# Kernel tuning notes

Measured on AMD Instinct MI355X. Metric: run time of the kernel, lower is better.

## Reference

```python
import jax, jax.numpy as jnp
import numpy as np

N_NODES = 100000
N_EDGES = 1600000
D_IN = 128
D_OUT = 128
NEG_SLOPE = 0.01  # torch F.leaky_relu default


def setup_inputs() -> dict:
    key = jax.random.key(0)
    k1, k2, k3, k4, k5 = jax.random.split(key, 5)
    h = jax.random.normal(k1, (N_NODES, D_IN), dtype=jnp.float32)
    # nn.Linear default init scale ~ 1/sqrt(fan_in)
    W = jax.random.normal(k2, (D_IN, D_OUT), dtype=jnp.float32) / np.sqrt(D_IN)
    attn_w = jax.random.normal(k3, (2 * D_OUT,), dtype=jnp.float32) / np.sqrt(2 * D_OUT)
    edge_src = jax.random.randint(k4, (N_EDGES,), 0, N_NODES, dtype=jnp.int32)
    edge_dst = jax.random.randint(k5, (N_EDGES,), 0, N_NODES, dtype=jnp.int32)
    return {"h": h, "W": W, "attn_w": attn_w, "edge_src": edge_src, "edge_dst": edge_dst}


def reference(h, W, attn_w, edge_src, edge_dst):
    n = h.shape[0]
    d = W.shape[1]
    z = h @ W                                   # [N, d]
    # attention_func(cat([z_src, z_dst])) == z_src @ a[:d] + z_dst @ a[d:]
    s_src = z @ attn_w[:d]                      # [N]
    s_dst = z @ attn_w[d:]                      # [N]
    e = jax.nn.leaky_relu(s_src[edge_src] + s_dst[edge_dst], NEG_SLOPE)  # [E]
    # segment softmax over incoming edges of each dst node
    m = jax.ops.segment_max(e, edge_dst, num_segments=n)   # [N], -inf for empty
    ex = jnp.exp(e - m[edge_dst])                           # [E]
    denom = jax.ops.segment_sum(ex, edge_dst, num_segments=n)  # [N]
    alpha = ex / denom[edge_dst]                             # [E]
    # weighted neighbor sum: sum_j alpha_ij * z_j
    out = jax.ops.segment_sum(alpha[:, None] * z[edge_src], edge_dst, num_segments=n)
    return out
```

## Files before the change

### kernel.cpp

```cpp
#include <hip/hip_runtime.h>

#define D 128
#define NEG_SLOPE 0.01f
#define BSHIFT 7
#define B1 1024
#define SCHUNK 4096
#define SLOT 2560

typedef __attribute__((ext_vector_type(8))) short short8;
typedef __attribute__((ext_vector_type(4))) float floatx4;

__device__ __forceinline__ unsigned f2bf_rne(float x) {
    unsigned u = __float_as_uint(x);
    return (u + 0x7fffu + ((u >> 16) & 1u)) >> 16;
}
#define BF_LO(u) __uint_as_float((u) << 16)
#define BF_HI(u) __uint_as_float((u) & 0xffff0000u)

__global__ void init_gcur(int* __restrict__ gcur) {
    const int i = threadIdx.x;
    gcur[i] = i * SLOT;
}

__global__ __launch_bounds__(256) void prep_wfrag(const float* __restrict__ W,
                                                  unsigned short* __restrict__ whi,
                                                  unsigned short* __restrict__ wlo) {
    const int idx = blockIdx.x * 256 + threadIdx.x;
    const int j    = idx & 7;
    const int lane = (idx >> 3) & 63;
    const int tk   = idx >> 9;
    const int kk = tk & 3, ct = tk >> 2;
    const int k = kk * 32 + (lane >> 4) * 8 + j;
    const int n = ct * 16 + (lane & 15);
    const float x = W[k * D + n];
    const unsigned hi = f2bf_rne(x);
    const float hf = __uint_as_float(hi << 16);
    whi[idx] = (unsigned short)hi;
    wlo[idx] = (unsigned short)(__float_as_uint(x - hf) >> 16);
}

__global__ __launch_bounds__(1024) void sort_scatter(const int* __restrict__ esrc,
                                                     const int* __restrict__ edst,
                                                     int* __restrict__ gcur,
                                                     int* __restrict__ pairs, int E) {
    __shared__ int cnt[B1], exc[B1], gbs[B1], cur[B1];
    __shared__ int spk[SCHUNK];
    __shared__ unsigned short sbkt[SCHUNK];
    const int t = threadIdx.x;
    cnt[t] = 0; cur[t] = 0;
    __syncthreads();

    const int e0 = blockIdx.x * SCHUNK;
    const int n  = min(SCHUNK, E - e0);

    int pk[4], bk[4];
#pragma unroll
    for (int k = 0; k < 4; ++k) {
        const int i = t + k * 1024;
        if (i < n) {
            const int d = edst[e0 + i];
            const int s = esrc[e0 + i];
            bk[k] = d >> BSHIFT;
            pk[k] = (s << BSHIFT) | (d & 127);
            atomicAdd(&cnt[bk[k]], 1);
        } else {
            bk[k] = -1;
        }
    }
    __syncthreads();

    exc[t] = cnt[t];
    __syncthreads();
    for (int off = 1; off < B1; off <<= 1) {
        int v = (t >= off) ? exc[t - off] : 0;
        __syncthreads();
        exc[t] += v;
        __syncthreads();
    }
    const int myexc = exc[t] - cnt[t];
    exc[t] = myexc;
    if (cnt[t] > 0) gbs[t] = atomicAdd(&gcur[t], cnt[t]);
    __syncthreads();

#pragma unroll
    for (int k = 0; k < 4; ++k) {
        if (bk[k] >= 0) {
            const int p = exc[bk[k]] + atomicAdd(&cur[bk[k]], 1);
            spk[p]  = pk[k];
            sbkt[p] = (unsigned short)bk[k];
        }
    }
    __syncthreads();

    for (int i = t; i < n; i += 1024) {
        const int b = sbkt[i];
        const int pos = gbs[b] + (i - exc[b]);
        if (pos < (b + 1) * SLOT) pairs[pos] = spk[i];
    }
}

__global__ __launch_bounds__(256) void fine_build(const int* __restrict__ pairs,
                                                  const int* __restrict__ gcur,
                                                  int* __restrict__ beg,
                                                  int* __restrict__ ncnt,
                                                  int* __restrict__ adj, int N) {
    __shared__ int cnt[128], sc[128], cur[128];
    const int b = blockIdx.x;
    const int base = b << BSHIFT;
    const int nd = min(128, N - base);
    const int t = threadIdx.x;
    const int s0 = b * SLOT;
    const int e1 = min(gcur[b], s0 + SLOT);
    if (t < 128) { cnt[t] = 0; cur[t] = 0; }
    __syncthreads();
    for (int i = s0 + t; i < e1; i += 256)
        atomicAdd(&cnt[pairs[i] & 127], 1);
    __syncthreads();
    if (t < 128) sc[t] = cnt[t];
    __syncthreads();
    for (int off = 1; off < 128; off <<= 1) {
        int v = (t < 128 && t >= off) ? sc[t - off] : 0;
        __syncthreads();
        if (t < 128) sc[t] += v;
        __syncthreads();
    }
    if (t < nd) {
        beg[base + t]  = s0 + sc[t] - cnt[t];
        ncnt[base + t] = cnt[t];
    }
    __syncthreads();
    for (int i = s0 + t; i < e1; i += 256) {
        const int pkv = pairs[i];
        const int d = pkv & 127;
        const int pos = s0 + (sc[d] - cnt[d]) + atomicAdd(&cur[d], 1);
        adj[pos] = pkv >> BSHIFT;
    }
}

__global__ __launch_bounds__(256) void gemm_zs(const float* __restrict__ h,
                                               const unsigned short* __restrict__ whi,
                                               const unsigned short* __restrict__ wlo,
                                               const float* __restrict__ aw,
                                               unsigned short* __restrict__ z,
                                               float* __restrict__ s_src,
                                               float* __restrict__ s_dst, int N) {
    const int t = threadIdx.x;
    const int lane = t & 63, quad = lane >> 4, l16 = lane & 15;
    const int rowbase = blockIdx.x * 64 + (t >> 6) * 16;
    const int arow = min(rowbase + l16, N - 1);
    const float* __restrict__ hrow = h + (size_t)arow * D;

    floatx4 acc[8];
#pragma unroll
    for (int ct = 0; ct < 8; ++ct) acc[ct] = (floatx4){0.f, 0.f, 0.f, 0.f};

#pragma unroll
    for (int kk = 0; kk < 4; ++kk) {
        const int k0 = kk * 32 + quad * 8;
        float4 x0 = *(const float4*)&hrow[k0];
        float4 x1 = *(const float4*)&hrow[k0 + 4];
        float xs[8] = {x0.x, x0.y, x0.z, x0.w, x1.x, x1.y, x1.z, x1.w};
        union { short8 v; unsigned short u[8]; } ahi, alo;
#pragma unroll
        for (int i = 0; i < 8; ++i) {
            unsigned hi = f2bf_rne(xs[i]);
            float hf = __uint_as_float(hi << 16);
            ahi.u[i] = (unsigned short)hi;
            alo.u[i] = (unsigned short)(__float_as_uint(xs[i] - hf) >> 16);
        }
#pragma unroll
        for (int ct = 0; ct < 8; ++ct) {
            const int fo = ((ct * 4 + kk) * 64 + lane) * 8;
            short8 bhi = *(const short8*)&whi[fo];
            short8 blo = *(const short8*)&wlo[fo];
            acc[ct] = __builtin_amdgcn_mfma_f32_16x16x32_bf16(ahi.v, bhi, acc[ct], 0, 0, 0);
            acc[ct] = __builtin_amdgcn_mfma_f32_16x16x32_bf16(alo.v, bhi, acc[ct], 0, 0, 0);
            acc[ct] = __builtin_amdgcn_mfma_f32_16x16x32_bf16(ahi.v, blo, acc[ct], 0, 0, 0);
        }
    }

#pragma unroll
    for (int ct = 0; ct < 8; ++ct)
#pragma unroll
        for (int reg = 0; reg < 4; ++reg) {
            int r = rowbase + quad * 4 + reg;
            if (r < N)
                z[(size_t)r * D + ct * 16 + l16] = (unsigned short)f2bf_rne(acc[ct][reg]);
        }

    float ps[4] = {0.f, 0.f, 0.f, 0.f}, pd[4] = {0.f, 0.f, 0.f, 0.f};
#pragma unroll
    for (int ct = 0; ct < 8; ++ct) {
        float as = aw[ct * 16 + l16];
        float ad = aw[128 + ct * 16 + l16];
#pragma unroll
        for (int reg = 0; reg < 4; ++reg) {
            ps[reg] = fmaf(acc[ct][reg], as, ps[reg]);
            pd[reg] = fmaf(acc[ct][reg], ad, pd[reg]);
        }
    }
#pragma unroll
    for (int reg = 0; reg < 4; ++reg)
#pragma unroll
        for (int o = 1; o < 16; o <<= 1) {
            ps[reg] += __shfl_xor(ps[reg], o, 64);
            pd[reg] += __shfl_xor(pd[reg], o, 64);
        }
    if (l16 == 0) {
#pragma unroll
        for (int reg = 0; reg < 4; ++reg) {
            int r = rowbase + quad * 4 + reg;
            if (r < N) { s_src[r] = ps[reg]; s_dst[r] = pd[reg]; }
        }
    }
}

__global__ __launch_bounds__(256) void aggregate(const unsigned short* __restrict__ z,
                                                 const float* __restrict__ s_src,
                                                 const float* __restrict__ s_dst,
                                                 const int* __restrict__ beg_,
                                                 const int* __restrict__ ncnt_,
                                                 const int* __restrict__ adj,
                                                 float* __restrict__ out, int N) {
    const int lane = threadIdx.x & 63;
    const int half = lane >> 5;
    const int l32  = lane & 31;
    const int q2   = l32 >> 4;
    const int l16  = lane & 15;
    const int hb   = half << 5;
    const int pairBase = blockIdx.x * 8 + (threadIdx.x >> 6) * 2;
    if (pairBase >= N) return;
    const int nodeA = pairBase, nodeB = pairBase + 1;
    const int cA = ncnt_[nodeA], bA = beg_[nodeA];
    int cB = 0, bB = 0;
    if (nodeB < N) { cB = ncnt_[nodeB]; bB = beg_[nodeB]; }

    auto fma8 = [&](float* ac, float w, const uint4& v) {
        ac[0] = fmaf(w, BF_LO(v.x), ac[0]); ac[1] = fmaf(w, BF_HI(v.x), ac[1]);
        ac[2] = fmaf(w, BF_LO(v.y), ac[2]); ac[3] = fmaf(w, BF_HI(v.y), ac[3]);
        ac[4] = fmaf(w, BF_LO(v.z), ac[4]); ac[5] = fmaf(w, BF_HI(v.z), ac[5]);
        ac[6] = fmaf(w, BF_LO(v.w), ac[6]); ac[7] = fmaf(w, BF_HI(v.w), ac[7]);
    };

    if (max(cA, cB) <= 32) {
        const int myn = pairBase + half;
        const int mb  = half ? bB : bA;
        const int mc  = half ? cB : cA;
        const float sd = s_dst[myn < N ? myn : 0];
        int s = 0; float e = -INFINITY;
        if (l32 < mc) {
            s = adj[mb + l32];
            float tt = s_src[s] + sd;
            e = (tt >= 0.f) ? tt : NEG_SLOPE * tt;
        }
        int sj[4]; uint4 zv[4];
#pragma unroll
        for (int u = 0; u < 4; ++u) sj[u] = __shfl(s, hb + u * 2 + q2, 64);
#pragma unroll
        for (int u = 0; u < 4; ++u)
            zv[u] = *(const uint4*)&z[(size_t)sj[u] * D + l16 * 8];

        float mx = e;
#pragma unroll
        for (int o = 16; o; o >>= 1) mx = fmaxf(mx, __shfl_xor(mx, o, 64));
        float ex = (l32 < mc) ? __expf(e - mx) : 0.f;
        float sum = ex;
#pragma unroll
        for (int o = 16; o; o >>= 1) sum += __shfl_xor(sum, o, 64);
        const float inv = (mc > 0) ? 1.f / sum : 0.f;
        const float w = ex * inv;

        float a[8] = {0.f,0.f,0.f,0.f,0.f,0.f,0.f,0.f};
        float bacc[8] = {0.f,0.f,0.f,0.f,0.f,0.f,0.f,0.f};
#pragma unroll
        for (int u = 0; u < 4; ++u) {
            const int ji = u * 2 + q2;
            float wj = __shfl(w, hb + ji, 64);
            wj = (ji < mc) ? wj : 0.f;
            fma8((u & 1) ? bacc : a, wj, zv[u]);
        }
        for (int jj = 8; jj < mc; jj += 8) {
            int ji2[4]; float wj[4]; int sj2[4];
#pragma unroll
            for (int u = 0; u < 4; ++u) {
                ji2[u] = jj + u * 2 + q2;
                wj[u]  = __shfl(w, hb + ji2[u], 64);
                sj2[u] = __shfl(s, hb + ji2[u], 64);
                wj[u]  = (ji2[u] < mc) ? wj[u] : 0.f;
            }
            uint4 z0 = *(const uint4*)&z[(size_t)sj2[0] * D + l16 * 8];
            uint4 z1 = *(const uint4*)&z[(size_t)sj2[1] * D + l16 * 8];
            uint4 z2 = *(const uint4*)&z[(size_t)sj2[2] * D + l16 * 8];
            uint4 z3 = *(const uint4*)&z[(size_t)sj2[3] * D + l16 * 8];
            fma8(a, wj[0], z0);
            fma8(bacc, wj[1], z1);
            fma8(a, wj[2], z2);
            fma8(bacc, wj[3], z3);
        }
#pragma unroll
        for (int i = 0; i < 8; ++i) {
            a[i] += bacc[i];
            a[i] += __shfl_xor(a[i], 16, 64);
        }
        if (q2 == 0 && myn < N) {
            float* o = &out[(size_t)myn * D + l16 * 8];
            *(float4*)o       = make_float4(a[0], a[1], a[2], a[3]);
            *(float4*)(o + 4) = make_float4(a[4], a[5], a[6], a[7]);
        }
        return;
    }

    const int q = lane >> 4;
    for (int which = 0; which < 2; ++which) {
        const int myn = which ? nodeB : nodeA;
        if (myn >= N) break;
        const int mb = which ? bB : bA;
        const int mc = which ? cB : cA;
        const float sd = s_dst[myn];
        float a[8] = {0.f,0.f,0.f,0.f,0.f,0.f,0.f,0.f};
        float bacc[8] = {0.f,0.f,0.f,0.f,0.f,0.f,0.f,0.f};
        float mx = -INFINITY;
        for (int j = lane; j < mc; j += 64) {
            float tt = s_src[adj[mb + j]] + sd;
            tt = (tt >= 0.f) ? tt : NEG_SLOPE * tt;
            mx = fmaxf(mx, tt);
        }
#pragma unroll
        for (int o = 32; o; o >>= 1) mx = fmaxf(mx, __shfl_xor(mx, o, 64));
        float sum = 0.f;
        for (int j = lane; j < mc; j += 64) {
            float tt = s_src[adj[mb + j]] + sd;
            tt = (tt >= 0.f) ? tt : NEG_SLOPE * tt;
            sum += __expf(tt - mx);
        }
#pragma unroll
        for (int o = 32; o; o >>= 1) sum += __shfl_xor(sum, o, 64);
        const float inv = (mc > 0) ? 1.f / sum : 0.f;
        for (int base2 = 0; base2 < mc; base2 += 64) {
            const int cc = min(64, mc - base2);
            int s = 0; float w = 0.f;
            if (lane < cc) {
                s = adj[mb + base2 + lane];
                float tt = s_src[s] + sd;
                tt = (tt >= 0.f) ? tt : NEG_SLOPE * tt;
                w = __expf(tt - mx) * inv;
            }
            for (int jj = 0; jj < cc; jj += 8) {
                const int ja = jj + q;
                const int jb = ja + 4;
                float wa = __shfl(w, ja, 64); int sa = __shfl(s, ja, 64);
                float wb = __shfl(w, jb, 64); int sb = __shfl(s, jb, 64);
                wa = (ja < cc) ? wa : 0.f;
                wb = (jb < cc) ? wb : 0.f;
                uint4 za = *(const uint4*)&z[(size_t)sa * D + l16 * 8];
                uint4 zb = *(const uint4*)&z[(size_t)sb * D + l16 * 8];
                fma8(a, wa, za);
                fma8(bacc, wb, zb);
            }
        }
#pragma unroll
        for (int i = 0; i < 8; ++i) {
            a[i] += bacc[i];
            a[i] += __shfl_xor(a[i], 16, 64);
            a[i] += __shfl_xor(a[i], 32, 64);
        }
        if (q == 0) {
            float* o = &out[(size_t)myn * D + l16 * 8];
            *(float4*)o       = make_float4(a[0], a[1], a[2], a[3]);
            *(float4*)(o + 4) = make_float4(a[4], a[5], a[6], a[7]);
        }
    }
}

extern "C" void kernel_launch(void* const* d_in, const int* in_sizes, int n_in,
                              void* d_out, int out_size, void* d_ws, size_t ws_size,
                              hipStream_t stream) {
    const float* h    = (const float*)d_in[0];
    const float* W    = (const float*)d_in[1];
    const float* aw   = (const float*)d_in[2];
    const int*   esrc = (const int*)d_in[3];
    const int*   edst = (const int*)d_in[4];
    float* out = (float*)d_out;

    const int N = in_sizes[0] / D;
    const int E = in_sizes[3];
    const int NB1   = (N + 127) >> BSHIFT;
    const int NSORT = (E + SCHUNK - 1) / SCHUNK;

    char* p = (char*)d_ws;
    auto carve = [&](size_t bytes) {
        void* r = (void*)p;
        p += (bytes + 255) & ~size_t(255);
        return r;
    };
    unsigned short* z = (unsigned short*)carve(size_t(N) * D * sizeof(unsigned short));
    float* s_src  = (float*)carve(size_t(N) * sizeof(float));
    float* s_dst  = (float*)carve(size_t(N) * sizeof(float));
    int*   pairs  = (int*)carve(size_t(NB1) * SLOT * sizeof(int));
    int*   adj    = (int*)carve(size_t(NB1) * SLOT * sizeof(int));
    int*   beg    = (int*)carve(size_t(N) * sizeof(int));
    int*   ncnt   = (int*)carve(size_t(N) * sizeof(int));
    int*   gcur   = (int*)carve(size_t(B1) * sizeof(int));
    unsigned short* whi = (unsigned short*)carve(16384 * sizeof(unsigned short));
    unsigned short* wlo = (unsigned short*)carve(16384 * sizeof(unsigned short));
    (void)ws_size; (void)n_in; (void)out_size;

    prep_wfrag<<<64, 256, 0, stream>>>(W, whi, wlo);
    init_gcur<<<1, B1, 0, stream>>>(gcur);
    sort_scatter<<<NSORT, 1024, 0, stream>>>(esrc, edst, gcur, pairs, E);
    fine_build<<<NB1, 256, 0, stream>>>(pairs, gcur, beg, ncnt, adj, N);
    gemm_zs<<<(N + 63) / 64, 256, 0, stream>>>(h, whi, wlo, aw, z, s_src, s_dst, N);
    aggregate<<<(N + 7) / 8, 256, 0, stream>>>(z, s_src, s_dst, beg, ncnt, adj, out, N);
}
```

Measured before the change: 222.4 us.

## Fold gcur init into prep kernel, use wave-shuffle scan, vectorize loads, split aggregate

Removes the separate init_gcur launch by having block 0 of prep_wfrag initialise the bucket cursors. In sort_scatter, each thread now loads four consecutive edges with int4 vector loads, and the barrier-heavy Hillis-Steele prefix scan is replaced by a wavefront shuffle scan plus a 16-entry cross-wave combine. The aggregate kernel is parameterised by a node range and launched twice over two halves of the nodes. The split adds a launch and seems to have no clear benefit.

```diff
diff --git a/kernel.cpp b/kernel.cpp
--- a/kernel.cpp
+++ b/kernel.cpp
@@ -17,14 +17,13 @@
 #define BF_LO(u) __uint_as_float((u) << 16)
 #define BF_HI(u) __uint_as_float((u) & 0xffff0000u)
 
-__global__ void init_gcur(int* __restrict__ gcur) {
-    const int i = threadIdx.x;
-    gcur[i] = i * SLOT;
-}
-
 __global__ __launch_bounds__(256) void prep_wfrag(const float* __restrict__ W,
                                                   unsigned short* __restrict__ whi,
-                                                  unsigned short* __restrict__ wlo) {
+                                                  unsigned short* __restrict__ wlo,
+                                                  int* __restrict__ gcur) {
+    if (blockIdx.x == 0) {
+        for (int i = threadIdx.x; i < B1; i += 256) gcur[i] = i * SLOT;
+    }
     const int idx = blockIdx.x * 256 + threadIdx.x;
     const int j    = idx & 7;
     const int lane = (idx >> 3) & 63;
@@ -46,7 +45,9 @@
     __shared__ int cnt[B1], exc[B1], gbs[B1], cur[B1];
     __shared__ int spk[SCHUNK];
     __shared__ unsigned short sbkt[SCHUNK];
+    __shared__ int wtot[16];
     const int t = threadIdx.x;
+    const int lane = t & 63, wv = t >> 6;
     cnt[t] = 0; cur[t] = 0;
     __syncthreads();
 
@@ -54,32 +55,49 @@
     const int n  = min(SCHUNK, E - e0);
 
     int pk[4], bk[4];
-#pragma unroll
-    for (int k = 0; k < 4; ++k) {
-        const int i = t + k * 1024;
-        if (i < n) {
-            const int d = edst[e0 + i];
-            const int s = esrc[e0 + i];
-            bk[k] = d >> BSHIFT;
-            pk[k] = (s << BSHIFT) | (d & 127);
+    const int i0 = t * 4;
+    if (i0 + 3 < n) {
+        const int4 dv = *(const int4*)&edst[e0 + i0];
+        const int4 sv = *(const int4*)&esrc[e0 + i0];
+        const int dd[4] = {dv.x, dv.y, dv.z, dv.w};
+        const int ss[4] = {sv.x, sv.y, sv.z, sv.w};
+#pragma unroll
+        for (int k = 0; k < 4; ++k) {
+            bk[k] = dd[k] >> BSHIFT;
+            pk[k] = (ss[k] << BSHIFT) | (dd[k] & 127);
             atomicAdd(&cnt[bk[k]], 1);
-        } else {
-            bk[k] = -1;
-        }
-    }
-    __syncthreads();
-
-    exc[t] = cnt[t];
-    __syncthreads();
-    for (int off = 1; off < B1; off <<= 1) {
-        int v = (t >= off) ? exc[t - off] : 0;
-        __syncthreads();
-        exc[t] += v;
-        __syncthreads();
-    }
-    const int myexc = exc[t] - cnt[t];
-    exc[t] = myexc;
-    if (cnt[t] > 0) gbs[t] = atomicAdd(&gcur[t], cnt[t]);
+        }
+    } else {
+#pragma unroll
+        for (int k = 0; k < 4; ++k) {
+            const int i = i0 + k;
+            if (i < n) {
+                const int d = edst[e0 + i];
+                const int s = esrc[e0 + i];
+                bk[k] = d >> BSHIFT;
+                pk[k] = (s << BSHIFT) | (d & 127);
+                atomicAdd(&cnt[bk[k]], 1);
+            } else {
+                bk[k] = -1;
+            }
+        }
+    }
+    __syncthreads();
+
+    const int c = cnt[t];
+    int incl = c;
+#pragma unroll
+    for (int o = 1; o < 64; o <<= 1) {
+        int v = __shfl_up(incl, o, 64);
+        if (lane >= o) incl += v;
+    }
+    if (lane == 63) wtot[wv] = incl;
+    __syncthreads();
+    int wpre = 0;
+#pragma unroll
+    for (int i = 0; i < 16; ++i) wpre += (i < wv) ? wtot[i] : 0;
+    exc[t] = wpre + incl - c;
+    if (c > 0) gbs[t] = atomicAdd(&gcur[t], c);
     __syncthreads();
 
 #pragma unroll
@@ -221,19 +239,20 @@
                                                  const int* __restrict__ beg_,
                                                  const int* __restrict__ ncnt_,
                                                  const int* __restrict__ adj,
-                                                 float* __restrict__ out, int N) {
+                                                 float* __restrict__ out,
+                                                 int nodeBase, int nEnd) {
     const int lane = threadIdx.x & 63;
     const int half = lane >> 5;
     const int l32  = lane & 31;
     const int q2   = l32 >> 4;
     const int l16  = lane & 15;
     const int hb   = half << 5;
-    const int pairBase = blockIdx.x * 8 + (threadIdx.x >> 6) * 2;
-    if (pairBase >= N) return;
+    const int pairBase = nodeBase + blockIdx.x * 8 + (threadIdx.x >> 6) * 2;
+    if (pairBase >= nEnd) return;
     const int nodeA = pairBase, nodeB = pairBase + 1;
     const int cA = ncnt_[nodeA], bA = beg_[nodeA];
     int cB = 0, bB = 0;
-    if (nodeB < N) { cB = ncnt_[nodeB]; bB = beg_[nodeB]; }
+    if (nodeB < nEnd) { cB = ncnt_[nodeB]; bB = beg_[nodeB]; }
 
     auto fma8 = [&](float* ac, float w, const uint4& v) {
         ac[0] = fmaf(w, BF_LO(v.x), ac[0]); ac[1] = fmaf(w, BF_HI(v.x), ac[1]);
@@ -244,9 +263,10 @@
 
     if (max(cA, cB) <= 32) {
         const int myn = pairBase + half;
+        const int valid = myn < nEnd;
         const int mb  = half ? bB : bA;
         const int mc  = half ? cB : cA;
-        const float sd = s_dst[myn < N ? myn : 0];
+        const float sd = s_dst[valid ? myn : 0];
         int s = 0; float e = -INFINITY;
         if (l32 < mc) {
             s = adj[mb + l32];
@@ -302,7 +322,7 @@
             a[i] += bacc[i];
             a[i] += __shfl_xor(a[i], 16, 64);
         }
-        if (q2 == 0 && myn < N) {
+        if (q2 == 0 && valid) {
             float* o = &out[(size_t)myn * D + l16 * 8];
             *(float4*)o       = make_float4(a[0], a[1], a[2], a[3]);
             *(float4*)(o + 4) = make_float4(a[4], a[5], a[6], a[7]);
@@ -313,7 +333,7 @@
     const int q = lane >> 4;
     for (int which = 0; which < 2; ++which) {
         const int myn = which ? nodeB : nodeA;
-        if (myn >= N) break;
+        if (myn >= nEnd) break;
         const int mb = which ? bB : bA;
         const int mc = which ? cB : cA;
         const float sd = s_dst[myn];
@@ -405,10 +425,11 @@
     unsigned short* wlo = (unsigned short*)carve(16384 * sizeof(unsigned short));
     (void)ws_size; (void)n_in; (void)out_size;
 
-    prep_wfrag<<<64, 256, 0, stream>>>(W, whi, wlo);
-    init_gcur<<<1, B1, 0, stream>>>(gcur);
+    prep_wfrag<<<64, 256, 0, stream>>>(W, whi, wlo, gcur);
     sort_scatter<<<NSORT, 1024, 0, stream>>>(esrc, edst, gcur, pairs, E);
     fine_build<<<NB1, 256, 0, stream>>>(pairs, gcur, beg, ncnt, adj, N);
     gemm_zs<<<(N + 63) / 64, 256, 0, stream>>>(h, whi, wlo, aw, z, s_src, s_dst, N);
-    aggregate<<<(N + 7) / 8, 256, 0, stream>>>(z, s_src, s_dst, beg, ncnt, adj, out, N);
-}
+    const int NH = (N / 2) & ~1;
+    aggregate<<<(NH + 7) / 8, 256, 0, stream>>>(z, s_src, s_dst, beg, ncnt, adj, out, 0, NH);
+    aggregate<<<(N - NH + 7) / 8, 256, 0, stream>>>(z, s_src, s_dst, beg, ncnt, adj, out, NH, N);
+}
```

After: 227.2 us. +2.2%, slower.
